# Performance work log

Hardware: AMD Instinct MI355X
Metric: run time of the kernel (lower is better)

## Reference

```python
import jax, jax.numpy as jnp
import numpy as np

N_QUBITS = 12
N_LAYERS = 16
DIM = 1 << N_QUBITS        # 4096
BATCH = 2048
N_CLASS = 5                # Z observables on wires 0..4

# --- static circuit structure (qubit 0 = most significant bit, DeepQuantum order) ---
_idx = np.arange(DIM)

def _cnot_perm(c, t):
    # CNOT(control=c, target=t): flip target bit where control bit is 1
    cbit = 1 << (N_QUBITS - 1 - c)
    tbit = 1 << (N_QUBITS - 1 - t)
    return np.where(_idx & cbit, _idx ^ tbit, _idx)

# cnot_ring: CNOT(q, (q+1) % n) for q = 0..n-1
CNOT_PERMS = [jnp.asarray(_cnot_perm(q, (q + 1) % N_QUBITS)) for q in range(N_QUBITS)]

# <Z_w> sign vectors for wires 0..4, stacked to (N_CLASS, DIM)
Z_SIGNS = jnp.asarray(
    np.stack([1.0 - 2.0 * ((_idx >> (N_QUBITS - 1 - w)) & 1) for w in range(N_CLASS)]).astype(np.float32)
)


def _apply_ry(psi, theta, q):
    """Apply RY(theta) on qubit q to batched state psi of shape (B, DIM)."""
    c = jnp.cos(theta / 2).astype(psi.real.dtype)
    s = jnp.sin(theta / 2).astype(psi.real.dtype)
    b = psi.shape[0]
    psi = psi.reshape(b, 1 << q, 2, 1 << (N_QUBITS - 1 - q))
    p0, p1 = psi[:, :, 0, :], psi[:, :, 1, :]
    out = jnp.stack([c * p0 - s * p1, s * p0 + c * p1], axis=2)
    return out.reshape(b, DIM)


def _circuit(psi, thetas):
    """num_layers x (RY layer + CNOT ring); returns (B, N_CLASS) Z expectations."""
    for l in range(N_LAYERS):
        for q in range(N_QUBITS):
            psi = _apply_ry(psi, thetas[l, q], q)
        for q in range(N_QUBITS):
            psi = psi[:, CNOT_PERMS[q]]
    probs = psi.real * psi.real + psi.imag * psi.imag  # (B, DIM)
    return probs @ Z_SIGNS.T                           # (B, N_CLASS)


def setup_inputs() -> dict:
    key = jax.random.key(0)
    k1, k2, k3, k4 = jax.random.split(key, 4)
    zr = jax.random.normal(k1, (BATCH, DIM), dtype=jnp.float32)
    zi = jax.random.normal(k2, (BATCH, DIM), dtype=jnp.float32)
    norm = jnp.sqrt(jnp.sum(zr * zr + zi * zi, axis=1, keepdims=True))  # valid quantum state
    zr, zi = zr / norm, zi / norm
    thetas = jax.random.normal(k3, (N_LAYERS, N_QUBITS), dtype=jnp.float32)
    y = jax.random.randint(k4, (BATCH,), 0, N_CLASS, dtype=jnp.int64)
    return {"z_real": zr, "z_imag": zi, "thetas": thetas, "y": y}


def reference(z_real, z_imag, thetas, y):
    psi = jax.lax.complex(z_real, z_imag)              # (B, 2**n) complex64
    output = _circuit(psi, thetas)                     # (B, N_CLASS) float32
    logp = jax.nn.log_softmax(output, axis=-1)
    nll = -jnp.take_along_axis(logp, y[:, None].astype(jnp.int32), axis=1)[:, 0]
    loss = jnp.mean(nll)                               # F.cross_entropy(output, y)
    return (loss, output)
```

## Files before the change

kernel.cpp:

```cpp
#include <hip/hip_runtime.h>
#include <math.h>


#define DIM     4096
#define NLAYERS 16
#define BATCH   2048
#define NCLASS  5

typedef float v2f __attribute__((ext_vector_type(2)));

__host__ __device__ constexpr unsigned gperm(unsigned i) {
  for (int q = 11; q >= 0; --q) {
    const unsigned cbit = 1u << (11 - q);
    const unsigned tbit = 1u << (11 - ((q + 1) % 12));
    if (i & cbit) i ^= tbit;
  }
  return i;
}
__host__ __device__ constexpr unsigned Qmap(unsigned lo) {
  return ((lo ^ (lo >> 3)) & 1u) | ((((lo >> 1) ^ (lo >> 3)) & 1u) << 1) |
         (((lo >> 2) & 1u) << 2) | ((lo & 1u) << 3);
}
__host__ __device__ constexpr unsigned Fmap(unsigned x) {
  return (x & 0xF00u) | ((x & 0xFu) << 4) | (((x >> 4) & 0xFu) ^ Qmap(x & 0xFu));
}

template<int CTRL>
__device__ __forceinline__ float dppf(float x) {
  return __int_as_float(__builtin_amdgcn_update_dpp(
      0, __float_as_int(x), CTRL, 0xF, 0xF, true));
}
template<int PAT>
__device__ __forceinline__ float swzf(float x) {
  return __int_as_float(__builtin_amdgcn_ds_swizzle(__float_as_int(x), PAT));
}

#define FOR16(M) M(0) M(1) M(2) M(3) M(4) M(5) M(6) M(7) M(8) M(9) M(10) \
  M(11) M(12) M(13) M(14) M(15)

#define ROT(i, j) {                                          \
    const v2f ti = p##i, tj = p##j;                          \
    p##i = __builtin_elementwise_fma(nkv, tj, ti);           \
    p##j = __builtin_elementwise_fma(kv,  ti, tj); }

#define GM8 ROT(0,8) ROT(1,9) ROT(2,10) ROT(3,11) ROT(4,12) ROT(5,13) \
  ROT(6,14) ROT(7,15)
#define GM4 ROT(0,4) ROT(1,5) ROT(2,6) ROT(3,7) ROT(8,12) ROT(9,13) \
  ROT(10,14) ROT(11,15)
#define GM2 ROT(0,2) ROT(1,3) ROT(4,6) ROT(5,7) ROT(8,10) ROT(9,11) \
  ROT(12,14) ROT(13,15)
#define GM1 ROT(0,1) ROT(2,3) ROT(4,5) ROT(6,7) ROT(8,9) ROT(10,11) \
  ROT(12,13) ROT(14,15)

#define GETK(g) \
  const float kG = __int_as_float(__builtin_amdgcn_readlane( \
      __float_as_int(vkg[(g) & 3]), l + (((g) >> 2) << 4)));

__global__ __launch_bounds__(256)
void qnn_sim(const float* __restrict__ zr, const float* __restrict__ zi,
             const float* __restrict__ thetas, const int* __restrict__ y,
             float* __restrict__ out) {
  __shared__ v2f buf2[DIM];
  const int b = blockIdx.x;
  const int t = threadIdx.x;

  const int w1b = (int)((((unsigned)t & 0xF0u) << 4) | ((unsigned)t & 0xFu));
  const int r1b = (int)Fmap((unsigned)t);
  const int Gt  = ((t << 4) ^ (t << 3)) & 0xFFF;
  const int r2b = (int)Fmap((unsigned)Gt);

  v2f p0,p1,p2,p3,p4,p5,p6,p7,p8,p9,p10,p11,p12,p13,p14,p15;
  {
    const float4* zr4 = (const float4*)(zr + (size_t)b * DIM + (t << 4));
    const float4* zi4 = (const float4*)(zi + (size_t)b * DIM + (t << 4));
    const float4 a0 = zr4[0], a1 = zr4[1], a2 = zr4[2], a3 = zr4[3];
    const float4 b0 = zi4[0], b1 = zi4[1], b2 = zi4[2], b3 = zi4[3];
    p0  = (v2f){a0.x, b0.x}; p1  = (v2f){a0.y, b0.y};
    p2  = (v2f){a0.z, b0.z}; p3  = (v2f){a0.w, b0.w};
    p4  = (v2f){a1.x, b1.x}; p5  = (v2f){a1.y, b1.y};
    p6  = (v2f){a1.z, b1.z}; p7  = (v2f){a1.w, b1.w};
    p8  = (v2f){a2.x, b2.x}; p9  = (v2f){a2.y, b2.y};
    p10 = (v2f){a2.z, b2.z}; p11 = (v2f){a2.w, b2.w};
    p12 = (v2f){a3.x, b3.x}; p13 = (v2f){a3.y, b3.y};
    p14 = (v2f){a3.z, b3.z}; p15 = (v2f){a3.w, b3.w};
  }

  float vkg[4];
  {
    const int lane = t & 63;
    if (lane < 48) {
      const int lsrc = lane & 15;
      const int gb = (lane >> 4) << 2;
#pragma unroll
      for (int j = 0; j < 4; ++j) {
        const float a = 0.5f * thetas[lsrc * 12 + gb + j];
        vkg[j] = sinf(a) / cosf(a);
      }
    } else {
      const int lsrc = lane - 48;
      float ca = 1.f, cb = 1.f;
      for (int g = 0; g < 4; ++g)  cb *= cosf(0.5f * thetas[lsrc * 12 + g]);
      for (int g = 4; g < 12; ++g) ca *= cosf(0.5f * thetas[lsrc * 12 + g]);
      vkg[0] = ca; vkg[1] = cb; vkg[2] = 0.f; vkg[3] = 0.f;
    }
  }

#pragma unroll 1
  for (int l = 0; l < NLAYERS; ++l) {
    const float CA = __int_as_float(__builtin_amdgcn_readlane(
        __float_as_int(vkg[0]), 48 + l));
    const float CB = __int_as_float(__builtin_amdgcn_readlane(
        __float_as_int(vkg[1]), 48 + l));

    { GETK(8)  const v2f kv = {kG,kG}, nkv = {-kG,-kG}; GM8 }
    { GETK(9)  const v2f kv = {kG,kG}, nkv = {-kG,-kG}; GM4 }
    { GETK(10) const v2f kv = {kG,kG}, nkv = {-kG,-kG}; GM2 }
    { GETK(11) const v2f kv = {kG,kG}, nkv = {-kG,-kG}; GM1 }

    {
      GETK(7)
      const float sg7 = (t & 1) ? kG : -kG;
      const v2f skv = {sg7,sg7};
#define DPPG7(i) { v2f pr; pr.x = dppf<0xB1>(p##i.x); pr.y = dppf<0xB1>(p##i.y); \
      p##i = __builtin_elementwise_fma(skv, pr, p##i); }
      FOR16(DPPG7)
#undef DPPG7
    }
    {
      GETK(6)
      const float sg6 = (t & 2) ? kG : -kG;
      const v2f skv = {sg6,sg6};
#define DPPG6(i) { v2f pr; pr.x = dppf<0x4E>(p##i.x); pr.y = dppf<0x4E>(p##i.y); \
      p##i = __builtin_elementwise_fma(skv, pr, p##i); }
      FOR16(DPPG6)
#undef DPPG6
    }
    {
      GETK(4)
      const float sg4 = (t & 8) ? kG : -kG;
      const v2f skv = {sg4,sg4};
#define DPPG4(i) { v2f pr; pr.x = dppf<0x128>(p##i.x); pr.y = dppf<0x128>(p##i.y); \
      p##i = __builtin_elementwise_fma(skv, pr, p##i); }
      FOR16(DPPG4)
#undef DPPG4
    }

    {
      GETK(5)
      const float sg5 = (t & 4) ? kG : -kG;
      const v2f skv = {sg5,sg5}, cav = {CA,CA};
#define SWG5(i) { v2f pr; pr.x = swzf<0x101F>(p##i.x); pr.y = swzf<0x101F>(p##i.y); \
      p##i = cav * __builtin_elementwise_fma(skv, pr, p##i); }
      FOR16(SWG5)
#undef SWG5
    }

    __syncthreads();
#define W1P(i) buf2[w1b ^ (int)Fmap((unsigned)i)] = p##i;
    FOR16(W1P)
#undef W1P
    __syncthreads();
#define R1P(i) p##i = buf2[r1b + (i << 8)];
    FOR16(R1P)
#undef R1P

    { GETK(0) const v2f kv = {kG,kG}, nkv = {-kG,-kG}; GM8 }
    { GETK(1) const v2f kv = {kG,kG}, nkv = {-kG,-kG}; GM4 }
    { GETK(2) const v2f kv = {kG,kG}, nkv = {-kG,-kG}; GM2 }
    { GETK(3) const v2f kv = {kG,kG}, nkv = {-kG,-kG}; GM1 }

    {
      const v2f cbv = {CB,CB};
#define SCB(i) p##i = cbv * p##i;
      FOR16(SCB)
#undef SCB
    }

#define W2P(i) buf2[r1b + (i << 8)] = p##i;
    FOR16(W2P)
#undef W2P
    __syncthreads();
#define R2P(i) p##i = buf2[r2b ^ (int)Fmap(gperm((unsigned)i))];
    FOR16(R2P)
#undef R2P
  }

  float P = 0.f;
#define ACC(i) P = __builtin_fmaf(p##i.x, p##i.x, P); \
               P = __builtin_fmaf(p##i.y, p##i.y, P);
  FOR16(ACC)
#undef ACC
  float e0 = ((t >> 7) & 1) ? -P : P;
  float e1 = ((t >> 6) & 1) ? -P : P;
  float e2 = ((t >> 5) & 1) ? -P : P;
  float e3 = ((t >> 4) & 1) ? -P : P;
  float e4 = ((t >> 3) & 1) ? -P : P;
#pragma unroll
  for (int off = 32; off >= 1; off >>= 1) {
    e0 += __shfl_xor(e0, off);
    e1 += __shfl_xor(e1, off);
    e2 += __shfl_xor(e2, off);
    e3 += __shfl_xor(e3, off);
    e4 += __shfl_xor(e4, off);
  }
  float* bf = (float*)buf2;
  __syncthreads();
  if ((t & 63) == 0) {
    const int w8 = (t >> 6) * 8;
    bf[w8 + 0] = e0; bf[w8 + 1] = e1; bf[w8 + 2] = e2;
    bf[w8 + 3] = e3; bf[w8 + 4] = e4;
  }
  __syncthreads();
  if (t == 0) {
    const float o0 = bf[0] + bf[8]  + bf[16] + bf[24];
    const float o1 = bf[1] + bf[9]  + bf[17] + bf[25];
    const float o2 = bf[2] + bf[10] + bf[18] + bf[26];
    const float o3 = bf[3] + bf[11] + bf[19] + bf[27];
    const float o4 = bf[4] + bf[12] + bf[20] + bf[28];
    float* op = out + 1 + (size_t)b * NCLASS;
    op[0] = o0; op[1] = o1; op[2] = o2; op[3] = o3; op[4] = o4;
    const float m = fmaxf(fmaxf(fmaxf(o0, o1), fmaxf(o2, o3)), o4);
    const float sum = expf(o0 - m) + expf(o1 - m) + expf(o2 - m) +
                      expf(o3 - m) + expf(o4 - m);
    const int yb = y[b];
    const float oy = (yb == 0) ? o0 : (yb == 1) ? o1 : (yb == 2) ? o2
                   : (yb == 3) ? o3 : o4;
    const float nll = (m + logf(sum)) - oy;
    atomicAdd(out, nll * (1.0f / BATCH));
  }
}

extern "C" void kernel_launch(void* const* d_in, const int* in_sizes, int n_in,
                              void* d_out, int out_size, void* d_ws, size_t ws_size,
                              hipStream_t stream) {
  const float* zr = (const float*)d_in[0];
  const float* zi = (const float*)d_in[1];
  const float* th = (const float*)d_in[2];
  const int*   y  = (const int*)d_in[3];
  float* out = (float*)d_out;
  hipMemsetAsync(out, 0, sizeof(float), stream);
  qnn_sim<<<BATCH, 256, 0, stream>>>(zr, zi, th, y, out);
}
```

Measured before the change: 217.3 us.

## Fuse next layer's qubit-5 rotation into LDS permutation read, merge cos scales

The swizzle-based qubit-5 RY rotation moves out of the loop. For the first layer it runs before the loop; for later layers it is folded into the post-CNOT LDS read by also loading the partner amplitude at address xor 6. The two per-layer cosine scale factors are merged into one product applied once per layer, and per-element LDS addresses are hoisted into precomputed registers. This removes 32 ds_swizzle ops per layer in exchange for 16 extra LDS reads and more live address registers, which may raise register pressure.

```diff
diff --git a/kernel.cpp b/kernel.cpp
--- a/kernel.cpp
+++ b/kernel.cpp
@@ -68,6 +68,12 @@
   const int r1b = (int)Fmap((unsigned)t);
   const int Gt  = ((t << 4) ^ (t << 3)) & 0xFFF;
   const int r2b = (int)Fmap((unsigned)Gt);
+
+#define MKADDR(i) \
+  const int w1a##i = w1b ^ (int)Fmap((unsigned)i); \
+  const int r2a##i = r2b ^ (int)Fmap(gperm((unsigned)i));
+  FOR16(MKADDR)
+#undef MKADDR
 
   v2f p0,p1,p2,p3,p4,p5,p6,p7,p8,p9,p10,p11,p12,p13,p14,p15;
   {
@@ -98,19 +104,27 @@
       }
     } else {
       const int lsrc = lane - 48;
-      float ca = 1.f, cb = 1.f;
-      for (int g = 0; g < 4; ++g)  cb *= cosf(0.5f * thetas[lsrc * 12 + g]);
-      for (int g = 4; g < 12; ++g) ca *= cosf(0.5f * thetas[lsrc * 12 + g]);
-      vkg[0] = ca; vkg[1] = cb; vkg[2] = 0.f; vkg[3] = 0.f;
-    }
+      float c = 1.f;
+      for (int g = 0; g < 12; ++g) c *= cosf(0.5f * thetas[lsrc * 12 + g]);
+      vkg[0] = c; vkg[1] = 0.f; vkg[2] = 0.f; vkg[3] = 0.f;
+    }
+  }
+
+  {
+    const float k5 = __int_as_float(__builtin_amdgcn_readlane(
+        __float_as_int(vkg[1]), 16));
+    const float sg5 = (t & 4) ? k5 : -k5;
+    const v2f skv = {sg5, sg5};
+#define SWG5(i) { v2f pr; pr.x = swzf<0x101F>(p##i.x); pr.y = swzf<0x101F>(p##i.y); \
+    p##i = __builtin_elementwise_fma(skv, pr, p##i); }
+    FOR16(SWG5)
+#undef SWG5
   }
 
 #pragma unroll 1
   for (int l = 0; l < NLAYERS; ++l) {
-    const float CA = __int_as_float(__builtin_amdgcn_readlane(
+    const float CL = __int_as_float(__builtin_amdgcn_readlane(
         __float_as_int(vkg[0]), 48 + l));
-    const float CB = __int_as_float(__builtin_amdgcn_readlane(
-        __float_as_int(vkg[1]), 48 + l));
 
     { GETK(8)  const v2f kv = {kG,kG}, nkv = {-kG,-kG}; GM8 }
     { GETK(9)  const v2f kv = {kG,kG}, nkv = {-kG,-kG}; GM4 }
@@ -145,18 +159,8 @@
 #undef DPPG4
     }
 
-    {
-      GETK(5)
-      const float sg5 = (t & 4) ? kG : -kG;
-      const v2f skv = {sg5,sg5}, cav = {CA,CA};
-#define SWG5(i) { v2f pr; pr.x = swzf<0x101F>(p##i.x); pr.y = swzf<0x101F>(p##i.y); \
-      p##i = cav * __builtin_elementwise_fma(skv, pr, p##i); }
-      FOR16(SWG5)
-#undef SWG5
-    }
-
     __syncthreads();
-#define W1P(i) buf2[w1b ^ (int)Fmap((unsigned)i)] = p##i;
+#define W1P(i) buf2[w1a##i] = p##i;
     FOR16(W1P)
 #undef W1P
     __syncthreads();
@@ -170,19 +174,30 @@
     { GETK(3) const v2f kv = {kG,kG}, nkv = {-kG,-kG}; GM1 }
 
     {
-      const v2f cbv = {CB,CB};
-#define SCB(i) p##i = cbv * p##i;
-      FOR16(SCB)
-#undef SCB
+      const v2f cv = {CL, CL};
+#define SCL(i) p##i = cv * p##i;
+      FOR16(SCL)
+#undef SCL
     }
 
 #define W2P(i) buf2[r1b + (i << 8)] = p##i;
     FOR16(W2P)
 #undef W2P
     __syncthreads();
-#define R2P(i) p##i = buf2[r2b ^ (int)Fmap(gperm((unsigned)i))];
+#define R2P(i) p##i = buf2[r2a##i];
     FOR16(R2P)
 #undef R2P
+
+    if (l < NLAYERS - 1) {
+      const float k5n = __int_as_float(__builtin_amdgcn_readlane(
+          __float_as_int(vkg[1]), (l + 1) + 16));
+      const float sg5 = (t & 4) ? k5n : -k5n;
+      const v2f skv = {sg5, sg5};
+#define R2F(i) { const v2f pr = buf2[r2a##i ^ 6]; \
+      p##i = __builtin_elementwise_fma(skv, pr, p##i); }
+      FOR16(R2F)
+#undef R2F
+    }
   }
 
   float P = 0.f;
```

Measured after the change: 215.2 us. No clear change (-1.0%).
